# Optimization experiments

Measured on AMD Instinct MI355X. Metric: run time of the kernel, lower is better.

The kernel has to match this reference:

```python
import jax, jax.numpy as jnp
import numpy as np

H = 768
L = 4096
P, KP = 8192, 8
EV, KE = 2048, 6
E = 16384
NR = 32
NUM_LABELS = 2


def setup_inputs() -> dict:
    key = jax.random.key(0)
    ks = jax.random.split(key, 10)
    seq = jax.random.normal(ks[0], (1, L, H), dtype=jnp.float32)
    phrase_idx = jax.random.randint(ks[1], (P, KP), 0, L, dtype=jnp.int32)
    phrase_mask = jnp.ones((P, KP), dtype=jnp.float32)
    event_idx = jax.random.randint(ks[2], (EV, KE), 0, L, dtype=jnp.int32)
    event_mask = jnp.ones((EV, KE), dtype=jnp.float32)
    pair_idx = jax.random.randint(ks[3], (E, 2), 0, EV, dtype=jnp.int32)
    root_idx = jax.random.randint(ks[4], (NR,), 0, P, dtype=jnp.int32)
    s1 = 1.0 / np.sqrt(2 * H)
    W1 = jax.random.normal(ks[5], (2 * H, H), dtype=jnp.float32) * s1
    b1 = jnp.zeros((H,), dtype=jnp.float32)
    Wb = jax.random.normal(ks[6], (2 * H, NUM_LABELS), dtype=jnp.float32) * s1
    bb = jnp.zeros((NUM_LABELS,), dtype=jnp.float32)
    return {"seq": seq, "phrase_idx": phrase_idx, "phrase_mask": phrase_mask,
            "event_idx": event_idx, "event_mask": event_mask, "pair_idx": pair_idx,
            "root_idx": root_idx, "W1": W1, "b1": b1, "Wb": Wb, "bb": bb}


def _masked_mean_gather(tok, idx, mask):
    # tok: [L,H]; idx: [N,K] int; mask: [N,K] float -> [N,H]
    g = tok[idx]                                  # [N,K,H] irregular gather
    s = jnp.einsum('nkh,nk->nh', g, mask)
    d = jnp.maximum(mask.sum(axis=1, keepdims=True), 1.0)
    return s / d


def reference(seq, phrase_idx, phrase_mask, event_idx, event_mask, pair_idx,
              root_idx, W1, b1, Wb, bb):
    tok = seq[0]                                   # [L,H] doc token embeddings
    # phrase embeddings: gather token indices per phrase, masked mean-pool
    ph = _masked_mean_gather(tok, phrase_idx, phrase_mask)   # [P,H]
    # event embeddings: gather span tokens per event, masked mean-pool
    ev = _masked_mean_gather(tok, event_idx, event_mask)     # [EV,H]
    # event-pair nodes: concat the two event embeddings, middle_layer MLP
    e1 = ev[pair_idx[:, 0]]                        # [E,H]
    e2 = ev[pair_idx[:, 1]]                        # [E,H]
    pairs = jnp.concatenate([e1, e2], axis=-1)     # [E,2H]
    node = jax.nn.relu(pairs @ W1 + b1)            # [E,H] (dropout inactive at eval)
    # virtual root: mean of sentence-root phrase embeddings
    vroot = ph[root_idx].mean(axis=0)              # [H]
    feat = jnp.concatenate([node, jnp.broadcast_to(vroot, node.shape)], axis=-1)
    logits = feat @ Wb + bb                        # [E,NUM_LABELS] bilinear classifier
    return logits
```

## Files before the change

### kernel.cpp

```cpp
#include <hip/hip_runtime.h>
#include <hip/hip_bf16.h>

#define H   768
#define H4  192
#define EVN 2048
#define KE  6
#define KP  8
#define EE  16384
#define NR  32

typedef __bf16 v8bf __attribute__((ext_vector_type(8)));
typedef float  v4f  __attribute__((ext_vector_type(4)));

__device__ __forceinline__ void gload16(const void* g, void* lds) {
    __builtin_amdgcn_global_load_lds(
        (const __attribute__((address_space(1))) void*)g,
        (__attribute__((address_space(3))) void*)lds, 16, 0, 0);
}
__device__ __forceinline__ float blo(unsigned u) {
    return __uint_as_float(u << 16);
}
__device__ __forceinline__ float bhi(unsigned u) {
    return __uint_as_float(u & 0xffff0000u);
}

__global__ __launch_bounds__(256) void pre_kernel(
    const float* __restrict__ seq,
    const int* __restrict__ eidx, const float* __restrict__ emask,
    const int* __restrict__ pidx, const float* __restrict__ pmask,
    const int* __restrict__ root_idx, const float* __restrict__ W1,
    __hip_bfloat16* __restrict__ evb, __hip_bfloat16* __restrict__ Wt,
    float* __restrict__ phr) {
    __shared__ float tile[64][65];
    const int b = blockIdx.x;
    const int t = threadIdx.x;
    const float4* seq4 = (const float4*)seq;

    if (b < 512) {
        const int w = t >> 6, l = t & 63;
        const int n = b * 4 + w;
        int idx[KE]; float mk[KE]; float ms = 0.f;
#pragma unroll
        for (int k = 0; k < KE; ++k) {
            idx[k] = eidx[n * KE + k];
            mk[k]  = emask[n * KE + k];
            ms    += mk[k];
        }
        const float inv = 1.f / fmaxf(ms, 1.f);
#pragma unroll
        for (int g = 0; g < 3; ++g) {
            const int t4 = l + g * 64;
            float4 acc = {0.f, 0.f, 0.f, 0.f};
#pragma unroll
            for (int k = 0; k < KE; ++k) {
                float4 v = seq4[idx[k] * H4 + t4];
                acc.x = fmaf(mk[k], v.x, acc.x);
                acc.y = fmaf(mk[k], v.y, acc.y);
                acc.z = fmaf(mk[k], v.z, acc.z);
                acc.w = fmaf(mk[k], v.w, acc.w);
            }
            __hip_bfloat16 o[4];
            o[0] = __float2bfloat16(acc.x * inv);
            o[1] = __float2bfloat16(acc.y * inv);
            o[2] = __float2bfloat16(acc.z * inv);
            o[3] = __float2bfloat16(acc.w * inv);
            *(uint2*)&evb[n * H + t4 * 4] = *(uint2*)o;
        }
    } else if (b < 520) {
        const int w = t >> 6, l = t & 63;
        const int r = (b - 512) * 4 + w;
        const int pr = root_idx[r];
        int idx[KP]; float mk[KP]; float ms = 0.f;
#pragma unroll
        for (int k = 0; k < KP; ++k) {
            idx[k] = pidx[pr * KP + k];
            mk[k]  = pmask[pr * KP + k];
            ms    += mk[k];
        }
        const float inv = 1.f / fmaxf(ms, 1.f);
#pragma unroll
        for (int g = 0; g < 3; ++g) {
            const int t4 = l + g * 64;
            float4 acc = {0.f, 0.f, 0.f, 0.f};
#pragma unroll
            for (int k = 0; k < KP; ++k) {
                float4 v = seq4[idx[k] * H4 + t4];
                acc.x = fmaf(mk[k], v.x, acc.x);
                acc.y = fmaf(mk[k], v.y, acc.y);
                acc.z = fmaf(mk[k], v.z, acc.z);
                acc.w = fmaf(mk[k], v.w, acc.w);
            }
            float4 o = {acc.x * inv, acc.y * inv, acc.z * inv, acc.w * inv};
            ((float4*)phr)[r * H4 + t4] = o;
        }
    } else {
        const int b2 = b - 520;
        const int k0 = (b2 % 12) * 64;
        const int j0 = (b2 / 12) * 64;
        const int s  = (j0 >= H) ? H : 0;
        const int n0 = j0 - s;
        const int c  = t & 63;
        const int r0 = t >> 6;
#pragma unroll
        for (int i = 0; i < 16; ++i) {
            const int r = r0 + i * 4;
            tile[r][c] = W1[(size_t)(s + k0 + r) * H + n0 + c];
        }
        __syncthreads();
#pragma unroll
        for (int i = 0; i < 16; ++i) {
            const int r = r0 + i * 4;
            Wt[(size_t)(j0 + r) * H + k0 + c] = __float2bfloat16(tile[c][r]);
        }
    }
}

__global__ __launch_bounds__(256) void gemm_kernel(
    const __hip_bfloat16* __restrict__ evb_,
    const __hip_bfloat16* __restrict__ Wt_,
    const float* __restrict__ b1v,
    const float* __restrict__ phr, const float* __restrict__ Wb,
    const float* __restrict__ bbv,
    __hip_bfloat16* __restrict__ evw, float* __restrict__ cvec) {
    __shared__ short As[3][8192];
    __shared__ short Bs[3][4096];

    if (blockIdx.x == 384) {
        float* r0s = (float*)&As[0][0];
        float* r1s = r0s + 256;
        const int t = threadIdx.x;
        float p0 = 0.f, p1 = 0.f;
#pragma unroll
        for (int w = 0; w < 3; ++w) {
            const int d = t + w * 256;
            float s = 0.f;
            for (int r = 0; r < NR; ++r) s += phr[r * H + d];
            const float v = s * (1.0f / NR);
            p0 = fmaf(v, Wb[(H + d) * 2 + 0], p0);
            p1 = fmaf(v, Wb[(H + d) * 2 + 1], p1);
        }
        r0s[t] = p0; r1s[t] = p1;
        __syncthreads();
        for (int off = 128; off > 0; off >>= 1) {
            if (t < off) { r0s[t] += r0s[t + off]; r1s[t] += r1s[t + off]; }
            __syncthreads();
        }
        if (t == 0) { cvec[0] = r0s[0] + bbv[0]; cvec[1] = r1s[0] + bbv[1]; }
        return;
    }

    const short* evb = (const short*)evb_;
    const short* Wt  = (const short*)Wt_;

    const int bid = blockIdx.x;
    const int swz = (bid & 7) * 48 + (bid >> 3);
    const int mt = swz / 24, nt = swz % 24;
    const int m0 = mt * 128, n0 = nt * 64;

    const int t = threadIdx.x;
    const int l = t & 63;
    const int w = t >> 6;
    const int wr = (w >> 1) * 64;
    const int wc = (w & 1) * 32;

    const short* aSrc[4]; int aOff[4];
#pragma unroll
    for (int c = 0; c < 4; ++c) {
        const int s = c * 256 + t;
        const int r = s >> 3, pg = s & 7, g = pg ^ (r & 7);
        aSrc[c] = evb + (size_t)(m0 + r) * H + g * 8;
        aOff[c] = s * 16;
    }
    const short* bSrc[2]; int bOff[2];
#pragma unroll
    for (int c = 0; c < 2; ++c) {
        const int s = c * 256 + t;
        const int r = s >> 3, pg = s & 7, g = pg ^ (r & 7);
        bSrc[c] = Wt + (size_t)(n0 + r) * H + g * 8;
        bOff[c] = s * 16;
    }

#define STAGE(tile, buf) do {                                              \
    _Pragma("unroll") for (int c_ = 0; c_ < 4; ++c_)                       \
        gload16(aSrc[c_] + (tile) * 64, (char*)As[buf] + aOff[c_]);        \
    _Pragma("unroll") for (int c_ = 0; c_ < 2; ++c_)                       \
        gload16(bSrc[c_] + (tile) * 64, (char*)Bs[buf] + bOff[c_]);        \
} while (0)

    const int fr = l & 15, gq = l >> 4, xm = fr & 7;
    int aRowB[4], bRowB[2];
#pragma unroll
    for (int mi = 0; mi < 4; ++mi) aRowB[mi] = (wr + mi * 16 + fr) * 128;
#pragma unroll
    for (int nj = 0; nj < 2; ++nj) bRowB[nj] = (wc + nj * 16 + fr) * 128;

    v4f acc[4][2] = {};

    STAGE(0, 0);
    STAGE(1, 1);

#pragma unroll
    for (int ks = 0; ks < 12; ++ks) {
        if (ks < 11) { asm volatile("s_waitcnt vmcnt(6)" ::: "memory"); }
        else         { asm volatile("s_waitcnt vmcnt(0)" ::: "memory"); }
        __builtin_amdgcn_sched_barrier(0);
        __builtin_amdgcn_s_barrier();
        __builtin_amdgcn_sched_barrier(0);
        if (ks < 10) STAGE(ks + 2, (ks + 2) % 3);
        const char* Ab = (const char*)As[ks % 3];
        const char* Bb = (const char*)Bs[ks % 3];
#pragma unroll
        for (int hh = 0; hh < 2; ++hh) {
            const int pgo = ((hh * 4 + gq) ^ xm) * 16;
            v8bf a0 = *(const v8bf*)(Ab + aRowB[0] + pgo);
            v8bf a1 = *(const v8bf*)(Ab + aRowB[1] + pgo);
            v8bf a2 = *(const v8bf*)(Ab + aRowB[2] + pgo);
            v8bf a3 = *(const v8bf*)(Ab + aRowB[3] + pgo);
            v8bf b0 = *(const v8bf*)(Bb + bRowB[0] + pgo);
            v8bf b1 = *(const v8bf*)(Bb + bRowB[1] + pgo);
            acc[0][0] = __builtin_amdgcn_mfma_f32_16x16x32_bf16(a0, b0, acc[0][0], 0, 0, 0);
            acc[0][1] = __builtin_amdgcn_mfma_f32_16x16x32_bf16(a0, b1, acc[0][1], 0, 0, 0);
            acc[1][0] = __builtin_amdgcn_mfma_f32_16x16x32_bf16(a1, b0, acc[1][0], 0, 0, 0);
            acc[1][1] = __builtin_amdgcn_mfma_f32_16x16x32_bf16(a1, b1, acc[1][1], 0, 0, 0);
            acc[2][0] = __builtin_amdgcn_mfma_f32_16x16x32_bf16(a2, b0, acc[2][0], 0, 0, 0);
            acc[2][1] = __builtin_amdgcn_mfma_f32_16x16x32_bf16(a2, b1, acc[2][1], 0, 0, 0);
            acc[3][0] = __builtin_amdgcn_mfma_f32_16x16x32_bf16(a3, b0, acc[3][0], 0, 0, 0);
            acc[3][1] = __builtin_amdgcn_mfma_f32_16x16x32_bf16(a3, b1, acc[3][1], 0, 0, 0);
        }
    }
#undef STAGE

    float bv[2];
#pragma unroll
    for (int nj = 0; nj < 2; ++nj) {
        const int ocol = n0 + wc + nj * 16 + fr;
        bv[nj] = (ocol >= H) ? b1v[ocol - H] : 0.f;
    }
#pragma unroll
    for (int mi = 0; mi < 4; ++mi)
#pragma unroll
        for (int nj = 0; nj < 2; ++nj) {
            const int ocol = n0 + wc + nj * 16 + fr;
#pragma unroll
            for (int r = 0; r < 4; ++r) {
                const int orow = m0 + wr + mi * 16 + gq * 4 + r;
                evw[(size_t)orow * 1536 + ocol] =
                    __float2bfloat16(acc[mi][nj][r] + bv[nj]);
            }
        }
}

__global__ __launch_bounds__(256) void pair_logits_kernel(
    const __hip_bfloat16* __restrict__ evw_, const int* __restrict__ pair_idx,
    const float* __restrict__ Wb, const float* __restrict__ cvec,
    float* __restrict__ out) {
    const ushort* evw = (const ushort*)evw_;
    const int wave = threadIdx.x >> 6;
    const int lane = threadIdx.x & 63;
    const int i = blockIdx.x * 4 + wave;
    const int p0 = pair_idx[i * 2 + 0];
    const int p1 = pair_idx[i * 2 + 1];
    const ushort* ra = evw + (size_t)p0 * 1536;
    const ushort* rb = evw + (size_t)p1 * 1536 + H;
    float acc0 = 0.f, acc1 = 0.f;
#pragma unroll
    for (int h = 0; h < 2; ++h) {
        const int j = h * 384 + lane * 6;
        uint3 ua = *(const uint3*)(ra + j);
        uint3 ub = *(const uint3*)(rb + j);
        float4 w0 = *(const float4*)(Wb + j * 2);
        float4 w1 = *(const float4*)(Wb + j * 2 + 4);
        float4 w2 = *(const float4*)(Wb + j * 2 + 8);
        float n0 = fmaxf(blo(ua.x) + blo(ub.x), 0.f);
        float n1 = fmaxf(bhi(ua.x) + bhi(ub.x), 0.f);
        float n2 = fmaxf(blo(ua.y) + blo(ub.y), 0.f);
        float n3 = fmaxf(bhi(ua.y) + bhi(ub.y), 0.f);
        float n4 = fmaxf(blo(ua.z) + blo(ub.z), 0.f);
        float n5 = fmaxf(bhi(ua.z) + bhi(ub.z), 0.f);
        acc0 += n0 * w0.x + n1 * w0.z + n2 * w1.x + n3 * w1.z + n4 * w2.x + n5 * w2.z;
        acc1 += n0 * w0.y + n1 * w0.w + n2 * w1.y + n3 * w1.w + n4 * w2.y + n5 * w2.w;
    }
#pragma unroll
    for (int off = 32; off > 0; off >>= 1) {
        acc0 += __shfl_xor(acc0, off, 64);
        acc1 += __shfl_xor(acc1, off, 64);
    }
    if (lane == 0) {
        out[i * 2 + 0] = acc0 + cvec[0];
        out[i * 2 + 1] = acc1 + cvec[1];
    }
}

extern "C" void kernel_launch(void* const* d_in, const int* in_sizes, int n_in,
                              void* d_out, int out_size, void* d_ws, size_t ws_size,
                              hipStream_t stream) {
    const float* seq         = (const float*)d_in[0];
    const int*   phrase_idx  = (const int*)  d_in[1];
    const float* phrase_mask = (const float*)d_in[2];
    const int*   event_idx   = (const int*)  d_in[3];
    const float* event_mask  = (const float*)d_in[4];
    const int*   pair_idx    = (const int*)  d_in[5];
    const int*   root_idx    = (const int*)  d_in[6];
    const float* W1          = (const float*)d_in[7];
    const float* b1          = (const float*)d_in[8];
    const float* Wb          = (const float*)d_in[9];
    const float* bb          = (const float*)d_in[10];
    float* out = (float*)d_out;

    char* wsb = (char*)d_ws;
    __hip_bfloat16* evb = (__hip_bfloat16*)wsb;
    __hip_bfloat16* Wt  = (__hip_bfloat16*)(wsb + 3145728);
    __hip_bfloat16* evw = (__hip_bfloat16*)(wsb + 5505024);
    float* phr = (float*)(wsb + 11796480);
    float* c   = (float*)(wsb + 11894784);

    pre_kernel<<<808, 256, 0, stream>>>(seq, event_idx, event_mask,
                                        phrase_idx, phrase_mask, root_idx,
                                        W1, evb, Wt, phr);
    gemm_kernel<<<385, 256, 0, stream>>>(evb, Wt, b1, phr, Wb, bb, evw, c);
    pair_logits_kernel<<<EE / 4, 256, 0, stream>>>(evw, pair_idx, Wb, c, out);
}
```

Before: 31.91 us.

## Fold root-vector dot into pre kernel and widen GEMM tile to 128x96

The pre kernel now computes each root phrase's masked-mean dot product with the Wb root half and writes 32 partial pairs. The pair-logits kernel reduces these partials per wave, which removes the extra root-reduction block from the GEMM and the phrase-embedding buffer round trip. The GEMM tile grows from 128x64 to 128x96, so the grid becomes 256 blocks, one per CU, with no tail and more MFMA reuse per A load. In exchange the GEMM uses more registers and LDS per block, and every pair-logits wave repeats the small reduction.

```diff
diff --git a/kernel.cpp b/kernel.cpp
--- a/kernel.cpp
+++ b/kernel.cpp
@@ -29,8 +29,9 @@
     const int* __restrict__ eidx, const float* __restrict__ emask,
     const int* __restrict__ pidx, const float* __restrict__ pmask,
     const int* __restrict__ root_idx, const float* __restrict__ W1,
+    const float* __restrict__ Wb,
     __hip_bfloat16* __restrict__ evb, __hip_bfloat16* __restrict__ Wt,
-    float* __restrict__ phr) {
+    float* __restrict__ dotr) {
     __shared__ float tile[64][65];
     const int b = blockIdx.x;
     const int t = threadIdx.x;
@@ -78,20 +79,33 @@
             ms    += mk[k];
         }
         const float inv = 1.f / fmaxf(ms, 1.f);
+        float p0 = 0.f, p1 = 0.f;
 #pragma unroll
         for (int g = 0; g < 3; ++g) {
             const int t4 = l + g * 64;
-            float4 acc = {0.f, 0.f, 0.f, 0.f};
+            float4 a = {0.f, 0.f, 0.f, 0.f};
 #pragma unroll
             for (int k = 0; k < KP; ++k) {
                 float4 v = seq4[idx[k] * H4 + t4];
-                acc.x = fmaf(mk[k], v.x, acc.x);
-                acc.y = fmaf(mk[k], v.y, acc.y);
-                acc.z = fmaf(mk[k], v.z, acc.z);
-                acc.w = fmaf(mk[k], v.w, acc.w);
+                a.x = fmaf(mk[k], v.x, a.x);
+                a.y = fmaf(mk[k], v.y, a.y);
+                a.z = fmaf(mk[k], v.z, a.z);
+                a.w = fmaf(mk[k], v.w, a.w);
             }
-            float4 o = {acc.x * inv, acc.y * inv, acc.z * inv, acc.w * inv};
-            ((float4*)phr)[r * H4 + t4] = o;
+            const int d = t4 * 4;
+            float4 q0 = *(const float4*)&Wb[(H + d) * 2];
+            float4 q1 = *(const float4*)&Wb[(H + d) * 2 + 4];
+            p0 += inv * (a.x * q0.x + a.y * q0.z + a.z * q1.x + a.w * q1.z);
+            p1 += inv * (a.x * q0.y + a.y * q0.w + a.z * q1.y + a.w * q1.w);
+        }
+#pragma unroll
+        for (int off = 32; off > 0; off >>= 1) {
+            p0 += __shfl_xor(p0, off, 64);
+            p1 += __shfl_xor(p1, off, 64);
+        }
+        if (l == 0) {
+            dotr[r * 2 + 0] = p0 * (1.0f / NR);
+            dotr[r * 2 + 1] = p1 * (1.0f / NR);
         }
     } else {
         const int b2 = b - 520;
@@ -119,49 +133,23 @@
     const __hip_bfloat16* __restrict__ evb_,
     const __hip_bfloat16* __restrict__ Wt_,
     const float* __restrict__ b1v,
-    const float* __restrict__ phr, const float* __restrict__ Wb,
-    const float* __restrict__ bbv,
-    __hip_bfloat16* __restrict__ evw, float* __restrict__ cvec) {
+    __hip_bfloat16* __restrict__ evw) {
     __shared__ short As[3][8192];
-    __shared__ short Bs[3][4096];
-
-    if (blockIdx.x == 384) {
-        float* r0s = (float*)&As[0][0];
-        float* r1s = r0s + 256;
-        const int t = threadIdx.x;
-        float p0 = 0.f, p1 = 0.f;
-#pragma unroll
-        for (int w = 0; w < 3; ++w) {
-            const int d = t + w * 256;
-            float s = 0.f;
-            for (int r = 0; r < NR; ++r) s += phr[r * H + d];
-            const float v = s * (1.0f / NR);
-            p0 = fmaf(v, Wb[(H + d) * 2 + 0], p0);
-            p1 = fmaf(v, Wb[(H + d) * 2 + 1], p1);
-        }
-        r0s[t] = p0; r1s[t] = p1;
-        __syncthreads();
-        for (int off = 128; off > 0; off >>= 1) {
-            if (t < off) { r0s[t] += r0s[t + off]; r1s[t] += r1s[t + off]; }
-            __syncthreads();
-        }
-        if (t == 0) { cvec[0] = r0s[0] + bbv[0]; cvec[1] = r1s[0] + bbv[1]; }
-        return;
-    }
+    __shared__ short Bs[3][6144];
 
     const short* evb = (const short*)evb_;
     const short* Wt  = (const short*)Wt_;
 
     const int bid = blockIdx.x;
-    const int swz = (bid & 7) * 48 + (bid >> 3);
-    const int mt = swz / 24, nt = swz % 24;
-    const int m0 = mt * 128, n0 = nt * 64;
+    const int swz = (bid & 7) * 32 + (bid >> 3);
+    const int mt = swz >> 4, nt = swz & 15;
+    const int m0 = mt * 128, n0 = nt * 96;
 
     const int t = threadIdx.x;
     const int l = t & 63;
     const int w = t >> 6;
     const int wr = (w >> 1) * 64;
-    const int wc = (w & 1) * 32;
+    const int wc = (w & 1) * 48;
 
     const short* aSrc[4]; int aOff[4];
 #pragma unroll
@@ -171,9 +159,9 @@
         aSrc[c] = evb + (size_t)(m0 + r) * H + g * 8;
         aOff[c] = s * 16;
     }
-    const short* bSrc[2]; int bOff[2];
-#pragma unroll
-    for (int c = 0; c < 2; ++c) {
+    const short* bSrc[3]; int bOff[3];
+#pragma unroll
+    for (int c = 0; c < 3; ++c) {
         const int s = c * 256 + t;
         const int r = s >> 3, pg = s & 7, g = pg ^ (r & 7);
         bSrc[c] = Wt + (size_t)(n0 + r) * H + g * 8;
@@ -183,25 +171,25 @@
 #define STAGE(tile, buf) do {                                              \
     _Pragma("unroll") for (int c_ = 0; c_ < 4; ++c_)                       \
         gload16(aSrc[c_] + (tile) * 64, (char*)As[buf] + aOff[c_]);        \
-    _Pragma("unroll") for (int c_ = 0; c_ < 2; ++c_)                       \
+    _Pragma("unroll") for (int c_ = 0; c_ < 3; ++c_)                       \
         gload16(bSrc[c_] + (tile) * 64, (char*)Bs[buf] + bOff[c_]);        \
 } while (0)
 
     const int fr = l & 15, gq = l >> 4, xm = fr & 7;
-    int aRowB[4], bRowB[2];
+    int aRowB[4], bRowB[3];
 #pragma unroll
     for (int mi = 0; mi < 4; ++mi) aRowB[mi] = (wr + mi * 16 + fr) * 128;
 #pragma unroll
-    for (int nj = 0; nj < 2; ++nj) bRowB[nj] = (wc + nj * 16 + fr) * 128;
-
-    v4f acc[4][2] = {};
+    for (int nj = 0; nj < 3; ++nj) bRowB[nj] = (wc + nj * 16 + fr) * 128;
+
+    v4f acc[4][3] = {};
 
     STAGE(0, 0);
     STAGE(1, 1);
 
 #pragma unroll
     for (int ks = 0; ks < 12; ++ks) {
-        if (ks < 11) { asm volatile("s_waitcnt vmcnt(6)" ::: "memory"); }
+        if (ks < 11) { asm volatile("s_waitcnt vmcnt(7)" ::: "memory"); }
         else         { asm volatile("s_waitcnt vmcnt(0)" ::: "memory"); }
         __builtin_amdgcn_sched_barrier(0);
         __builtin_amdgcn_s_barrier();
@@ -218,28 +206,33 @@
             v8bf a3 = *(const v8bf*)(Ab + aRowB[3] + pgo);
             v8bf b0 = *(const v8bf*)(Bb + bRowB[0] + pgo);
             v8bf b1 = *(const v8bf*)(Bb + bRowB[1] + pgo);
+            v8bf b2 = *(const v8bf*)(Bb + bRowB[2] + pgo);
             acc[0][0] = __builtin_amdgcn_mfma_f32_16x16x32_bf16(a0, b0, acc[0][0], 0, 0, 0);
             acc[0][1] = __builtin_amdgcn_mfma_f32_16x16x32_bf16(a0, b1, acc[0][1], 0, 0, 0);
+            acc[0][2] = __builtin_amdgcn_mfma_f32_16x16x32_bf16(a0, b2, acc[0][2], 0, 0, 0);
             acc[1][0] = __builtin_amdgcn_mfma_f32_16x16x32_bf16(a1, b0, acc[1][0], 0, 0, 0);
             acc[1][1] = __builtin_amdgcn_mfma_f32_16x16x32_bf16(a1, b1, acc[1][1], 0, 0, 0);
+            acc[1][2] = __builtin_amdgcn_mfma_f32_16x16x32_bf16(a1, b2, acc[1][2], 0, 0, 0);
             acc[2][0] = __builtin_amdgcn_mfma_f32_16x16x32_bf16(a2, b0, acc[2][0], 0, 0, 0);
             acc[2][1] = __builtin_amdgcn_mfma_f32_16x16x32_bf16(a2, b1, acc[2][1], 0, 0, 0);
+            acc[2][2] = __builtin_amdgcn_mfma_f32_16x16x32_bf16(a2, b2, acc[2][2], 0, 0, 0);
             acc[3][0] = __builtin_amdgcn_mfma_f32_16x16x32_bf16(a3, b0, acc[3][0], 0, 0, 0);
             acc[3][1] = __builtin_amdgcn_mfma_f32_16x16x32_bf16(a3, b1, acc[3][1], 0, 0, 0);
+            acc[3][2] = __builtin_amdgcn_mfma_f32_16x16x32_bf16(a3, b2, acc[3][2], 0, 0, 0);
         }
     }
 #undef STAGE
 
-    float bv[2];
-#pragma unroll
-    for (int nj = 0; nj < 2; ++nj) {
+    float bv[3];
+#pragma unroll
+    for (int nj = 0; nj < 3; ++nj) {
         const int ocol = n0 + wc + nj * 16 + fr;
         bv[nj] = (ocol >= H) ? b1v[ocol - H] : 0.f;
     }
 #pragma unroll
     for (int mi = 0; mi < 4; ++mi)
 #pragma unroll
-        for (int nj = 0; nj < 2; ++nj) {
+        for (int nj = 0; nj < 3; ++nj) {
             const int ocol = n0 + wc + nj * 16 + fr;
 #pragma unroll
             for (int r = 0; r < 4; ++r) {
@@ -252,11 +245,21 @@
 
 __global__ __launch_bounds__(256) void pair_logits_kernel(
     const __hip_bfloat16* __restrict__ evw_, const int* __restrict__ pair_idx,
-    const float* __restrict__ Wb, const float* __restrict__ cvec,
-    float* __restrict__ out) {
+    const float* __restrict__ Wb, const float* __restrict__ dotr,
+    const float* __restrict__ bbv, float* __restrict__ out) {
     const ushort* evw = (const ushort*)evw_;
     const int wave = threadIdx.x >> 6;
     const int lane = threadIdx.x & 63;
+
+    float c0 = 0.f, c1 = 0.f;
+    if (lane < 32) { c0 = dotr[lane * 2]; c1 = dotr[lane * 2 + 1]; }
+#pragma unroll
+    for (int off = 32; off > 0; off >>= 1) {
+        c0 += __shfl_xor(c0, off, 64);
+        c1 += __shfl_xor(c1, off, 64);
+    }
+    c0 += bbv[0]; c1 += bbv[1];
+
     const int i = blockIdx.x * 4 + wave;
     const int p0 = pair_idx[i * 2 + 0];
     const int p1 = pair_idx[i * 2 + 1];
@@ -286,8 +289,8 @@
         acc1 += __shfl_xor(acc1, off, 64);
     }
     if (lane == 0) {
-        out[i * 2 + 0] = acc0 + cvec[0];
-        out[i * 2 + 1] = acc1 + cvec[1];
+        out[i * 2 + 0] = acc0 + c0;
+        out[i * 2 + 1] = acc1 + c1;
     }
 }
 
@@ -311,12 +314,12 @@
     __hip_bfloat16* evb = (__hip_bfloat16*)wsb;
     __hip_bfloat16* Wt  = (__hip_bfloat16*)(wsb + 3145728);
     __hip_bfloat16* evw = (__hip_bfloat16*)(wsb + 5505024);
-    float* phr = (float*)(wsb + 11796480);
-    float* c   = (float*)(wsb + 11894784);
+    float* dotr = (float*)(wsb + 11796480);
 
     pre_kernel<<<808, 256, 0, stream>>>(seq, event_idx, event_mask,
                                         phrase_idx, phrase_mask, root_idx,
-                                        W1, evb, Wt, phr);
-    gemm_kernel<<<385, 256, 0, stream>>>(evb, Wt, b1, phr, Wb, bb, evw, c);
-    pair_logits_kernel<<<EE / 4, 256, 0, stream>>>(evw, pair_idx, Wb, c, out);
-}
+                                        W1, Wb, evb, Wt, dotr);
+    gemm_kernel<<<256, 256, 0, stream>>>(evb, Wt, b1, evw);
+    pair_logits_kernel<<<EE / 4, 256, 0, stream>>>(evw, pair_idx, Wb, dotr,
+                                                   bb, out);
+}
```

Result: slower. 33.89 us (+6.2%).
